# Performance work log

Hardware: AMD Instinct MI355X
Metric: run time of the kernel (lower is better)

Reference implementation:

```python
import jax, jax.numpy as jnp
import numpy as np

N_HEADS = 4
D_K = 64
SCALE = D_K ** (-0.5)


def setup_inputs() -> dict:
    key = jax.random.key(0)
    k1, k2, k3, k4, k5 = jax.random.split(key, 5)
    B, C, H, W = 16, 256, 32, 32
    x = jax.random.normal(k1, (B, C, H, W), dtype=jnp.float32)
    # Linear weights stored as (in, out) for x @ W convention
    w_qkv = jax.random.normal(k2, (C, N_HEADS * D_K * 3), dtype=jnp.float32) * (C ** -0.5)
    b_qkv = jax.random.normal(k3, (N_HEADS * D_K * 3,), dtype=jnp.float32) * 0.02
    w_out = jax.random.normal(k4, (N_HEADS * D_K, C), dtype=jnp.float32) * ((N_HEADS * D_K) ** -0.5)
    b_out = jax.random.normal(k5, (C,), dtype=jnp.float32) * 0.02
    return {"x": x, "w_qkv": w_qkv, "b_qkv": b_qkv, "w_out": w_out, "b_out": b_out}


def reference(x, w_qkv, b_qkv, w_out, b_out):
    # NOTE: the original torch module defines GroupNorm but never applies it
    # in forward; we faithfully reproduce the forward as written.
    B, C, H, W = x.shape
    S = H * W
    xs = x.reshape(B, C, S).transpose(0, 2, 1)            # [B, S, C]
    qkv = (xs @ w_qkv + b_qkv).reshape(B, S, N_HEADS, 3 * D_K)
    q, k, v = jnp.split(qkv, 3, axis=-1)                   # each [B, S, H, d_k]
    attn = jnp.einsum('bihd,bjhd->bijh', q, k) * SCALE     # [B, S, S, H]
    attn = jax.nn.softmax(attn, axis=2)                    # softmax over j (keys)
    res = jnp.einsum('bijh,bjhd->bihd', attn, v)           # [B, S, H, d_k]
    res = res.reshape(B, S, N_HEADS * D_K)
    res = res @ w_out + b_out + xs                         # residual add
    return res.transpose(0, 2, 1).reshape(B, C, H, W)
```

## Files before the change

### kernel.cpp

```cpp
#include <hip/hip_runtime.h>
#include <hip/hip_bf16.h>

typedef __attribute__((ext_vector_type(8))) short short8;
typedef __attribute__((ext_vector_type(4))) short short4v;
typedef __attribute__((ext_vector_type(4))) float floatx4;
typedef unsigned short u16;

#define SCL_LOG2E 0.1803368801111204f

__device__ inline u16 f2b(float f) {
  __hip_bfloat16 h = __float2bfloat16(f);
  union { __hip_bfloat16 h; u16 u; } cv; cv.h = h; return cv.u;
}
__device__ inline float b2f(u16 u) {
  union { u16 u; __hip_bfloat16 h; } cv; cv.u = u; return __bfloat162float(cv.h);
}

__global__ __launch_bounds__(256) void tr_f32_bf16(const float* __restrict__ in,
                                                   u16* __restrict__ out, int R, int Cc) {
  __shared__ u16 tile[32][33];
  int bz = blockIdx.z;
  const float* inb = in + (size_t)bz * R * Cc;
  u16* outb = out + (size_t)bz * R * Cc;
  int c0 = blockIdx.x * 32, r0 = blockIdx.y * 32;
  int tx = threadIdx.x, ty = threadIdx.y;
#pragma unroll
  for (int i = 0; i < 32; i += 8)
    tile[ty + i][tx] = f2b(inb[(size_t)(r0 + ty + i) * Cc + c0 + tx]);
  __syncthreads();
#pragma unroll
  for (int i = 0; i < 32; i += 8)
    outb[(size_t)(c0 + ty + i) * R + r0 + tx] = tile[tx][ty + i];
}

__global__ __launch_bounds__(256) void tr64_f32_bf16(const float* __restrict__ in,
                                                     u16* __restrict__ out,
                                                     int R, int Cc) {
  __shared__ u16 tile[64][72];
  int bz = blockIdx.z;
  const float* inb = in + (size_t)bz * R * Cc;
  u16* outb = out + (size_t)bz * R * Cc;
  int c0 = blockIdx.x * 64, r0 = blockIdx.y * 64;
  int tx = threadIdx.x, ty = threadIdx.y;
#pragma unroll
  for (int i = 0; i < 4; i++) {
    int r = ty + 16 * i;
    float4 v = *(const float4*)&inb[(size_t)(r0 + r) * Cc + c0 + tx * 4];
    tile[tx * 4 + 0][r] = f2b(v.x);
    tile[tx * 4 + 1][r] = f2b(v.y);
    tile[tx * 4 + 2][r] = f2b(v.z);
    tile[tx * 4 + 3][r] = f2b(v.w);
  }
  __syncthreads();
#pragma unroll
  for (int i = 0; i < 4; i++) {
    int cc = ty + 16 * i;
    ushort4 o = *(ushort4*)&tile[cc][tx * 4];
    *(ushort4*)&outb[(size_t)(c0 + cc) * R + r0 + tx * 4] = o;
  }
}

__global__ __launch_bounds__(256) void qkv_gemm(const u16* __restrict__ xs,
                                                const u16* __restrict__ wT,
                                                const float* __restrict__ bias,
                                                u16* __restrict__ Qo,
                                                u16* __restrict__ Ko,
                                                u16* __restrict__ Vto) {
  __shared__ u16 As[128 * 32];
  __shared__ u16 Bs[128 * 32];
  const int tid = threadIdx.x, wave = tid >> 6, lane = tid & 63;
  const int l15 = lane & 15, quad = lane >> 4;
  const int wm = (wave >> 1) * 64, wn = (wave & 1) * 64;
  const int m0 = blockIdx.x * 128, n0 = blockIdx.y * 128;

  floatx4 acc[4][4] = {};
  const int srow = wave * 32 + (lane >> 2);
  const int scol = (lane & 3) * 8;

  for (int kt = 0; kt < 256; kt += 32) {
#pragma unroll
    for (int i = 0; i < 2; i++) {
      int r = srow + i * 16;
      *(short8*)&As[r * 32 + scol] =
          *(const short8*)&xs[(size_t)(m0 + r) * 256 + kt + scol];
      *(short8*)&Bs[r * 32 + scol] =
          *(const short8*)&wT[(size_t)(n0 + r) * 256 + kt + scol];
    }
    __syncthreads();
    short8 af[4], bfr[4];
#pragma unroll
    for (int mi = 0; mi < 4; mi++)
      af[mi] = *(short8*)&As[(wm + mi * 16 + l15) * 32 + quad * 8];
#pragma unroll
    for (int ni = 0; ni < 4; ni++)
      bfr[ni] = *(short8*)&Bs[(wn + ni * 16 + l15) * 32 + quad * 8];
#pragma unroll
    for (int mi = 0; mi < 4; mi++)
#pragma unroll
      for (int ni = 0; ni < 4; ni++)
        acc[mi][ni] = __builtin_amdgcn_mfma_f32_16x16x32_bf16(af[mi], bfr[ni],
                                                              acc[mi][ni], 0, 0, 0);
    __syncthreads();
  }

#pragma unroll
  for (int ni = 0; ni < 4; ni++) {
    int n = n0 + wn + ni * 16 + l15;
    float bv = bias[n];
    int h = n / 192;
    int rem = n - h * 192;
#pragma unroll
    for (int mi = 0; mi < 4; mi++) {
      int gm = m0 + wm + mi * 16 + quad * 4;
      int bb = gm >> 10, s = gm & 1023;
      if (rem < 128) {
        u16* dst;
        float scl;
        if (rem < 64) { dst = Qo; scl = SCL_LOG2E; } else { dst = Ko; scl = 1.0f; }
        int d = rem & 63;
#pragma unroll
        for (int r = 0; r < 4; r++)
          dst[((size_t)(bb * 4 + h) * 1024 + s + r) * 64 + d] =
              f2b((acc[mi][ni][r] + bv) * scl);
      } else {
        int d = rem - 128;
        ushort4 pk;
        pk.x = f2b(acc[mi][ni][0] + bv);
        pk.y = f2b(acc[mi][ni][1] + bv);
        pk.z = f2b(acc[mi][ni][2] + bv);
        pk.w = f2b(acc[mi][ni][3] + bv);
        *(ushort4*)&Vto[((size_t)(bb * 4 + h) * 64 + d) * 1024 + s] = pk;
      }
    }
  }
}

__global__ __launch_bounds__(256, 4) void attn_kern(const u16* __restrict__ Q,
                                                    const u16* __restrict__ K,
                                                    const u16* __restrict__ Vt,
                                                    u16* __restrict__ O) {
  __shared__ u16 kv[2 * 2 * 64 * 72];
  const int bh = blockIdx.y;
  const u16* Qp = Q + (size_t)bh * 64 * 1024;
  const u16* Kp = K + (size_t)bh * 64 * 1024;
  const u16* Vp = Vt + (size_t)bh * 64 * 1024;
  u16* Op = O + (size_t)bh * 64 * 1024;
  const int q0 = blockIdx.x * 64;
  const int tid = threadIdx.x, wave = tid >> 6, lane = tid & 63;
  const int l15 = lane & 15, quad = lane >> 4;

  short8 qa[2];
#pragma unroll
  for (int ks = 0; ks < 2; ks++)
    qa[ks] = *(const short8*)&Qp[(size_t)(q0 + wave * 16 + l15) * 64 + ks * 32 + quad * 8];

  const int srow = tid >> 2;
  const int sc = (tid & 3) * 16;

  {
    short8 k0 = *(const short8*)&Kp[(size_t)srow * 64 + sc];
    short8 k1 = *(const short8*)&Kp[(size_t)srow * 64 + sc + 8];
    short8 v0 = *(const short8*)&Vp[(size_t)srow * 1024 + sc];
    short8 v1 = *(const short8*)&Vp[(size_t)srow * 1024 + sc + 8];
    *(short8*)&kv[srow * 72 + sc] = k0;
    *(short8*)&kv[srow * 72 + sc + 8] = k1;
    *(short8*)&kv[4608 + srow * 72 + sc] = v0;
    *(short8*)&kv[4608 + srow * 72 + sc + 8] = v1;
  }
  __syncthreads();

  float lsum = 0.f;
  floatx4 acc[4] = {};

  for (int t = 0; t < 16; t++) {
    const u16* Ksb = kv + (t & 1) * 9216;
    const u16* Vsb = Ksb + 4608;

    short8 nk0, nk1, nv0, nv1;
    if (t < 15) {
      nk0 = *(const short8*)&Kp[(size_t)((t + 1) * 64 + srow) * 64 + sc];
      nk1 = *(const short8*)&Kp[(size_t)((t + 1) * 64 + srow) * 64 + sc + 8];
      nv0 = *(const short8*)&Vp[(size_t)srow * 1024 + (t + 1) * 64 + sc];
      nv1 = *(const short8*)&Vp[(size_t)srow * 1024 + (t + 1) * 64 + sc + 8];
    }

    floatx4 sf[4];
#pragma unroll
    for (int mj = 0; mj < 4; mj++) {
      short8 kb0 = *(const short8*)&Ksb[(mj * 16 + l15) * 72 + quad * 8];
      short8 kb1 = *(const short8*)&Ksb[(mj * 16 + l15) * 72 + 32 + quad * 8];
      floatx4 z = {};
      z = __builtin_amdgcn_mfma_f32_16x16x32_bf16(kb0, qa[0], z, 0, 0, 0);
      sf[mj] = __builtin_amdgcn_mfma_f32_16x16x32_bf16(kb1, qa[1], z, 0, 0, 0);
    }

    short4v pb[4];
#pragma unroll
    for (int mj = 0; mj < 4; mj++) {
      float p0 = exp2f(sf[mj][0]), p1 = exp2f(sf[mj][1]);
      float p2 = exp2f(sf[mj][2]), p3 = exp2f(sf[mj][3]);
      lsum += (p0 + p1) + (p2 + p3);
      short4v pk;
      pk[0] = (short)f2b(p0); pk[1] = (short)f2b(p1);
      pk[2] = (short)f2b(p2); pk[3] = (short)f2b(p3);
      pb[mj] = pk;
    }

#pragma unroll
    for (int c = 0; c < 4; c++)
#pragma unroll
      for (int md = 0; md < 4; md++) {
        short4v va = *(const short4v*)&Vsb[(md * 16 + l15) * 72 + c * 16 + quad * 4];
        acc[md] = __builtin_amdgcn_mfma_f32_16x16x16bf16_1k(va, pb[c], acc[md], 0, 0, 0);
      }

    if (t < 15) {
      u16* dst = kv + ((t + 1) & 1) * 9216;
      *(short8*)&dst[srow * 72 + sc] = nk0;
      *(short8*)&dst[srow * 72 + sc + 8] = nk1;
      *(short8*)&dst[4608 + srow * 72 + sc] = nv0;
      *(short8*)&dst[4608 + srow * 72 + sc + 8] = nv1;
    }
    __syncthreads();
  }

  lsum += __shfl_xor(lsum, 16, 64);
  lsum += __shfl_xor(lsum, 32, 64);
  float inv = 1.f / lsum;

  __syncthreads();
  u16* Ot = kv;
#pragma unroll
  for (int md = 0; md < 4; md++) {
    uint2 pk;
    u16 a0 = f2b(acc[md][0] * inv), a1 = f2b(acc[md][1] * inv);
    u16 a2 = f2b(acc[md][2] * inv), a3 = f2b(acc[md][3] * inv);
    pk.x = (unsigned)a0 | ((unsigned)a1 << 16);
    pk.y = (unsigned)a2 | ((unsigned)a3 << 16);
    *(uint2*)&Ot[(wave * 16 + l15) * 72 + md * 16 + quad * 4] = pk;
  }
#pragma unroll
  for (int h = 0; h < 2; h++) {
    int row = h * 8 + (lane >> 3);
    int col = (lane & 7) * 8;
    short8 v = *(const short8*)&Ot[(wave * 16 + row) * 72 + col];
    *(short8*)&Op[(size_t)(q0 + wave * 16 + row) * 64 + col] = v;
  }
}

__global__ __launch_bounds__(256) void out_gemm(const u16* __restrict__ Oin,
                                                const u16* __restrict__ wT,
                                                const float* __restrict__ bias,
                                                const float* __restrict__ x,
                                                float* __restrict__ out) {
  __shared__ u16 As[128 * 32];
  __shared__ u16 Bs[128 * 32];
  const int tid = threadIdx.x, wave = tid >> 6, lane = tid & 63;
  const int l15 = lane & 15, quad = lane >> 4;
  const int wm = (wave >> 1) * 64, wn = (wave & 1) * 64;
  const int m0 = blockIdx.x * 128, n0 = blockIdx.y * 128;
  const int bb = m0 >> 10;

  floatx4 acc[4][4] = {};
  const int srow = wave * 32 + (lane >> 2);
  const int scol = (lane & 3) * 8;

  for (int kt = 0; kt < 256; kt += 32) {
    int h = kt >> 6, d0 = kt & 63;
#pragma unroll
    for (int i = 0; i < 2; i++) {
      int r = srow + i * 16;
      int s = (m0 + r) & 1023;
      *(short8*)&As[r * 32 + scol] =
          *(const short8*)&Oin[((size_t)(bb * 4 + h) * 1024 + s) * 64 + d0 + scol];
      *(short8*)&Bs[r * 32 + scol] =
          *(const short8*)&wT[(size_t)(n0 + r) * 256 + kt + scol];
    }
    __syncthreads();
    short8 af[4], bfr[4];
#pragma unroll
    for (int mi = 0; mi < 4; mi++)
      af[mi] = *(short8*)&As[(wm + mi * 16 + l15) * 32 + quad * 8];
#pragma unroll
    for (int ni = 0; ni < 4; ni++)
      bfr[ni] = *(short8*)&Bs[(wn + ni * 16 + l15) * 32 + quad * 8];
#pragma unroll
    for (int mi = 0; mi < 4; mi++)
#pragma unroll
      for (int ni = 0; ni < 4; ni++)
        acc[mi][ni] = __builtin_amdgcn_mfma_f32_16x16x32_bf16(af[mi], bfr[ni],
                                                              acc[mi][ni], 0, 0, 0);
    __syncthreads();
  }

#pragma unroll
  for (int ni = 0; ni < 4; ni++) {
    int c = n0 + wn + ni * 16 + l15;
    float bv = bias[c];
#pragma unroll
    for (int mi = 0; mi < 4; mi++) {
      int gm = m0 + wm + mi * 16 + quad * 4;
      int s = gm & 1023;
      size_t idx = ((size_t)bb * 256 + c) * 1024 + s;
      float4 xr = *(const float4*)&x[idx];
      float4 o;
      o.x = acc[mi][ni][0] + bv + xr.x;
      o.y = acc[mi][ni][1] + bv + xr.y;
      o.z = acc[mi][ni][2] + bv + xr.z;
      o.w = acc[mi][ni][3] + bv + xr.w;
      *(float4*)&out[idx] = o;
    }
  }
}

extern "C" void kernel_launch(void* const* d_in, const int* in_sizes, int n_in,
                              void* d_out, int out_size, void* d_ws, size_t ws_size,
                              hipStream_t stream) {
  const float* x     = (const float*)d_in[0];
  const float* w_qkv = (const float*)d_in[1];
  const float* b_qkv = (const float*)d_in[2];
  const float* w_out = (const float*)d_in[3];
  const float* b_out = (const float*)d_in[4];
  float* out = (float*)d_out;
  char* ws = (char*)d_ws;

  u16* xs    = (u16*)(ws);
  u16* wqkvT = (u16*)(ws + 8388608);
  u16* woutT = (u16*)(ws + 8388608 + 393216);
  u16* Qb    = (u16*)(ws + 8912896);
  u16* Kb    = (u16*)(ws + 8912896 + 8388608);
  u16* Vtb   = (u16*)(ws + 8912896 + 16777216);
  u16* Ob    = xs;

  tr64_f32_bf16<<<dim3(16, 4, 16), dim3(16, 16), 0, stream>>>(x, xs, 256, 1024);
  tr_f32_bf16<<<dim3(24, 8, 1), dim3(32, 8), 0, stream>>>(w_qkv, wqkvT, 256, 768);
  tr_f32_bf16<<<dim3(8, 8, 1), dim3(32, 8), 0, stream>>>(w_out, woutT, 256, 256);
  qkv_gemm<<<dim3(128, 6), 256, 0, stream>>>(xs, wqkvT, b_qkv, Qb, Kb, Vtb);
  attn_kern<<<dim3(16, 64), 256, 0, stream>>>(Qb, Kb, Vtb, Ob);
  out_gemm<<<dim3(128, 2), 256, 0, stream>>>(Ob, woutT, b_out, x, out);
}
```

Before: 145.0 us.

## Fuse fp32-to-bf16 transposes into GEMMs and double per-wave query rows in attention

Removes the three standalone transpose/convert kernels. The QKV and output GEMMs now read fp32 x and the weights directly, converting to bf16 and transposing into padded shared memory inside the load loop. The attention kernel now processes 32 query rows per wave (128 per block), so each K/V tile loaded into LDS is reused for twice as many queries; launch bounds drop to 2 blocks per SM. The output GEMM uses 64-row tiles to launch more blocks. In exchange, more registers are used in attention, and GEMM loads become scalar LDS scatter stores that may hit bank conflicts.

```diff
diff --git a/kernel.cpp b/kernel.cpp
--- a/kernel.cpp
+++ b/kernel.cpp
@@ -12,88 +12,49 @@
   __hip_bfloat16 h = __float2bfloat16(f);
   union { __hip_bfloat16 h; u16 u; } cv; cv.h = h; return cv.u;
 }
-__device__ inline float b2f(u16 u) {
-  union { u16 u; __hip_bfloat16 h; } cv; cv.u = u; return __bfloat162float(cv.h);
-}
-
-__global__ __launch_bounds__(256) void tr_f32_bf16(const float* __restrict__ in,
-                                                   u16* __restrict__ out, int R, int Cc) {
-  __shared__ u16 tile[32][33];
-  int bz = blockIdx.z;
-  const float* inb = in + (size_t)bz * R * Cc;
-  u16* outb = out + (size_t)bz * R * Cc;
-  int c0 = blockIdx.x * 32, r0 = blockIdx.y * 32;
-  int tx = threadIdx.x, ty = threadIdx.y;
-#pragma unroll
-  for (int i = 0; i < 32; i += 8)
-    tile[ty + i][tx] = f2b(inb[(size_t)(r0 + ty + i) * Cc + c0 + tx]);
-  __syncthreads();
-#pragma unroll
-  for (int i = 0; i < 32; i += 8)
-    outb[(size_t)(c0 + ty + i) * R + r0 + tx] = tile[tx][ty + i];
-}
-
-__global__ __launch_bounds__(256) void tr64_f32_bf16(const float* __restrict__ in,
-                                                     u16* __restrict__ out,
-                                                     int R, int Cc) {
-  __shared__ u16 tile[64][72];
-  int bz = blockIdx.z;
-  const float* inb = in + (size_t)bz * R * Cc;
-  u16* outb = out + (size_t)bz * R * Cc;
-  int c0 = blockIdx.x * 64, r0 = blockIdx.y * 64;
-  int tx = threadIdx.x, ty = threadIdx.y;
-#pragma unroll
-  for (int i = 0; i < 4; i++) {
-    int r = ty + 16 * i;
-    float4 v = *(const float4*)&inb[(size_t)(r0 + r) * Cc + c0 + tx * 4];
-    tile[tx * 4 + 0][r] = f2b(v.x);
-    tile[tx * 4 + 1][r] = f2b(v.y);
-    tile[tx * 4 + 2][r] = f2b(v.z);
-    tile[tx * 4 + 3][r] = f2b(v.w);
-  }
-  __syncthreads();
-#pragma unroll
-  for (int i = 0; i < 4; i++) {
-    int cc = ty + 16 * i;
-    ushort4 o = *(ushort4*)&tile[cc][tx * 4];
-    *(ushort4*)&outb[(size_t)(c0 + cc) * R + r0 + tx * 4] = o;
-  }
-}
-
-__global__ __launch_bounds__(256) void qkv_gemm(const u16* __restrict__ xs,
-                                                const u16* __restrict__ wT,
+
+__global__ __launch_bounds__(256) void qkv_gemm(const float* __restrict__ x,
+                                                const float* __restrict__ wq,
                                                 const float* __restrict__ bias,
                                                 u16* __restrict__ Qo,
                                                 u16* __restrict__ Ko,
                                                 u16* __restrict__ Vto) {
-  __shared__ u16 As[128 * 32];
-  __shared__ u16 Bs[128 * 32];
+  __shared__ u16 As[128 * 40];
+  __shared__ u16 Bs[128 * 40];
   const int tid = threadIdx.x, wave = tid >> 6, lane = tid & 63;
   const int l15 = lane & 15, quad = lane >> 4;
   const int wm = (wave >> 1) * 64, wn = (wave & 1) * 64;
   const int m0 = blockIdx.x * 128, n0 = blockIdx.y * 128;
+  const int bb = m0 >> 10, s0 = m0 & 1023;
+  const int cl = tid >> 3, u = tid & 7;
 
   floatx4 acc[4][4] = {};
-  const int srow = wave * 32 + (lane >> 2);
-  const int scol = (lane & 3) * 8;
 
   for (int kt = 0; kt < 256; kt += 32) {
-#pragma unroll
-    for (int i = 0; i < 2; i++) {
-      int r = srow + i * 16;
-      *(short8*)&As[r * 32 + scol] =
-          *(const short8*)&xs[(size_t)(m0 + r) * 256 + kt + scol];
-      *(short8*)&Bs[r * 32 + scol] =
-          *(const short8*)&wT[(size_t)(n0 + r) * 256 + kt + scol];
+    const float* xr = x + ((size_t)(bb * 256 + kt + cl)) * 1024 + s0;
+    const float* wr = wq + (size_t)(kt + cl) * 768 + n0;
+#pragma unroll
+    for (int j = 0; j < 4; j++) {
+      int e = u * 4 + 32 * j;
+      float4 va = *(const float4*)&xr[e];
+      float4 vb = *(const float4*)&wr[e];
+      As[(e + 0) * 40 + cl] = f2b(va.x);
+      As[(e + 1) * 40 + cl] = f2b(va.y);
+      As[(e + 2) * 40 + cl] = f2b(va.z);
+      As[(e + 3) * 40 + cl] = f2b(va.w);
+      Bs[(e + 0) * 40 + cl] = f2b(vb.x);
+      Bs[(e + 1) * 40 + cl] = f2b(vb.y);
+      Bs[(e + 2) * 40 + cl] = f2b(vb.z);
+      Bs[(e + 3) * 40 + cl] = f2b(vb.w);
     }
     __syncthreads();
     short8 af[4], bfr[4];
 #pragma unroll
     for (int mi = 0; mi < 4; mi++)
-      af[mi] = *(short8*)&As[(wm + mi * 16 + l15) * 32 + quad * 8];
+      af[mi] = *(short8*)&As[(wm + mi * 16 + l15) * 40 + quad * 8];
 #pragma unroll
     for (int ni = 0; ni < 4; ni++)
-      bfr[ni] = *(short8*)&Bs[(wn + ni * 16 + l15) * 32 + quad * 8];
+      bfr[ni] = *(short8*)&Bs[(wn + ni * 16 + l15) * 40 + quad * 8];
 #pragma unroll
     for (int mi = 0; mi < 4; mi++)
 #pragma unroll
@@ -112,7 +73,7 @@
 #pragma unroll
     for (int mi = 0; mi < 4; mi++) {
       int gm = m0 + wm + mi * 16 + quad * 4;
-      int bb = gm >> 10, s = gm & 1023;
+      int s = gm & 1023;
       if (rem < 128) {
         u16* dst;
         float scl;
@@ -135,7 +96,7 @@
   }
 }
 
-__global__ __launch_bounds__(256, 4) void attn_kern(const u16* __restrict__ Q,
+__global__ __launch_bounds__(256, 2) void attn_kern(const u16* __restrict__ Q,
                                                     const u16* __restrict__ K,
                                                     const u16* __restrict__ Vt,
                                                     u16* __restrict__ O) {
@@ -145,14 +106,17 @@
   const u16* Kp = K + (size_t)bh * 64 * 1024;
   const u16* Vp = Vt + (size_t)bh * 64 * 1024;
   u16* Op = O + (size_t)bh * 64 * 1024;
-  const int q0 = blockIdx.x * 64;
+  const int q0 = blockIdx.x * 128;
   const int tid = threadIdx.x, wave = tid >> 6, lane = tid & 63;
   const int l15 = lane & 15, quad = lane >> 4;
 
-  short8 qa[2];
-#pragma unroll
-  for (int ks = 0; ks < 2; ks++)
-    qa[ks] = *(const short8*)&Qp[(size_t)(q0 + wave * 16 + l15) * 64 + ks * 32 + quad * 8];
+  short8 qa[2][2];
+#pragma unroll
+  for (int qi = 0; qi < 2; qi++)
+#pragma unroll
+    for (int kh = 0; kh < 2; kh++)
+      qa[qi][kh] = *(const short8*)&Qp[(size_t)(q0 + wave * 32 + qi * 16 + l15) * 64 +
+                                       kh * 32 + quad * 8];
 
   const int srow = tid >> 2;
   const int sc = (tid & 3) * 16;
@@ -169,8 +133,8 @@
   }
   __syncthreads();
 
-  float lsum = 0.f;
-  floatx4 acc[4] = {};
+  float lsum[2] = {0.f, 0.f};
+  floatx4 acc[2][4] = {};
 
   for (int t = 0; t < 16; t++) {
     const u16* Ksb = kv + (t & 1) * 9216;
@@ -184,34 +148,48 @@
       nv1 = *(const short8*)&Vp[(size_t)srow * 1024 + (t + 1) * 64 + sc + 8];
     }
 
-    floatx4 sf[4];
-#pragma unroll
-    for (int mj = 0; mj < 4; mj++) {
-      short8 kb0 = *(const short8*)&Ksb[(mj * 16 + l15) * 72 + quad * 8];
-      short8 kb1 = *(const short8*)&Ksb[(mj * 16 + l15) * 72 + 32 + quad * 8];
-      floatx4 z = {};
-      z = __builtin_amdgcn_mfma_f32_16x16x32_bf16(kb0, qa[0], z, 0, 0, 0);
-      sf[mj] = __builtin_amdgcn_mfma_f32_16x16x32_bf16(kb1, qa[1], z, 0, 0, 0);
-    }
-
-    short4v pb[4];
-#pragma unroll
-    for (int mj = 0; mj < 4; mj++) {
-      float p0 = exp2f(sf[mj][0]), p1 = exp2f(sf[mj][1]);
-      float p2 = exp2f(sf[mj][2]), p3 = exp2f(sf[mj][3]);
-      lsum += (p0 + p1) + (p2 + p3);
-      short4v pk;
-      pk[0] = (short)f2b(p0); pk[1] = (short)f2b(p1);
-      pk[2] = (short)f2b(p2); pk[3] = (short)f2b(p3);
-      pb[mj] = pk;
-    }
+    short8 kb[4][2];
+#pragma unroll
+    for (int mj = 0; mj < 4; mj++)
+#pragma unroll
+      for (int kh = 0; kh < 2; kh++)
+        kb[mj][kh] = *(const short8*)&Ksb[(mj * 16 + l15) * 72 + kh * 32 + quad * 8];
+
+    floatx4 sf[2][4];
+#pragma unroll
+    for (int qi = 0; qi < 2; qi++)
+#pragma unroll
+      for (int mj = 0; mj < 4; mj++) {
+        floatx4 z = {};
+        z = __builtin_amdgcn_mfma_f32_16x16x32_bf16(kb[mj][0], qa[qi][0], z, 0, 0, 0);
+        sf[qi][mj] =
+            __builtin_amdgcn_mfma_f32_16x16x32_bf16(kb[mj][1], qa[qi][1], z, 0, 0, 0);
+      }
+
+    short4v pb[2][4];
+#pragma unroll
+    for (int qi = 0; qi < 2; qi++)
+#pragma unroll
+      for (int mj = 0; mj < 4; mj++) {
+        float p0 = exp2f(sf[qi][mj][0]), p1 = exp2f(sf[qi][mj][1]);
+        float p2 = exp2f(sf[qi][mj][2]), p3 = exp2f(sf[qi][mj][3]);
+        lsum[qi] += (p0 + p1) + (p2 + p3);
+        short4v pk;
+        pk[0] = (short)f2b(p0); pk[1] = (short)f2b(p1);
+        pk[2] = (short)f2b(p2); pk[3] = (short)f2b(p3);
+        pb[qi][mj] = pk;
+      }
 
 #pragma unroll
     for (int c = 0; c < 4; c++)
 #pragma unroll
       for (int md = 0; md < 4; md++) {
         short4v va = *(const short4v*)&Vsb[(md * 16 + l15) * 72 + c * 16 + quad * 4];
-        acc[md] = __builtin_amdgcn_mfma_f32_16x16x16bf16_1k(va, pb[c], acc[md], 0, 0, 0);
+#pragma unroll
+        for (int qi = 0; qi < 2; qi++)
+          acc[qi][md] =
+              __builtin_amdgcn_mfma_f32_16x16x16bf16_1k(va, pb[qi][c], acc[qi][md],
+                                                        0, 0, 0);
       }
 
     if (t < 15) {
@@ -224,68 +202,78 @@
     __syncthreads();
   }
 
-  lsum += __shfl_xor(lsum, 16, 64);
-  lsum += __shfl_xor(lsum, 32, 64);
-  float inv = 1.f / lsum;
+  float inv[2];
+#pragma unroll
+  for (int qi = 0; qi < 2; qi++) {
+    lsum[qi] += __shfl_xor(lsum[qi], 16, 64);
+    lsum[qi] += __shfl_xor(lsum[qi], 32, 64);
+    inv[qi] = 1.f / lsum[qi];
+  }
 
   __syncthreads();
   u16* Ot = kv;
 #pragma unroll
-  for (int md = 0; md < 4; md++) {
-    uint2 pk;
-    u16 a0 = f2b(acc[md][0] * inv), a1 = f2b(acc[md][1] * inv);
-    u16 a2 = f2b(acc[md][2] * inv), a3 = f2b(acc[md][3] * inv);
-    pk.x = (unsigned)a0 | ((unsigned)a1 << 16);
-    pk.y = (unsigned)a2 | ((unsigned)a3 << 16);
-    *(uint2*)&Ot[(wave * 16 + l15) * 72 + md * 16 + quad * 4] = pk;
-  }
-#pragma unroll
-  for (int h = 0; h < 2; h++) {
-    int row = h * 8 + (lane >> 3);
+  for (int qi = 0; qi < 2; qi++)
+#pragma unroll
+    for (int md = 0; md < 4; md++) {
+      uint2 pk;
+      u16 a0 = f2b(acc[qi][md][0] * inv[qi]), a1 = f2b(acc[qi][md][1] * inv[qi]);
+      u16 a2 = f2b(acc[qi][md][2] * inv[qi]), a3 = f2b(acc[qi][md][3] * inv[qi]);
+      pk.x = (unsigned)a0 | ((unsigned)a1 << 16);
+      pk.y = (unsigned)a2 | ((unsigned)a3 << 16);
+      *(uint2*)&Ot[(wave * 32 + qi * 16 + l15) * 72 + md * 16 + quad * 4] = pk;
+    }
+  __syncthreads();
+#pragma unroll
+  for (int rr = 0; rr < 4; rr++) {
+    int row = wave * 32 + (lane >> 3) + 8 * rr;
     int col = (lane & 7) * 8;
-    short8 v = *(const short8*)&Ot[(wave * 16 + row) * 72 + col];
-    *(short8*)&Op[(size_t)(q0 + wave * 16 + row) * 64 + col] = v;
+    short8 v = *(const short8*)&Ot[row * 72 + col];
+    *(short8*)&Op[(size_t)(q0 + row) * 64 + col] = v;
   }
 }
 
 __global__ __launch_bounds__(256) void out_gemm(const u16* __restrict__ Oin,
-                                                const u16* __restrict__ wT,
+                                                const float* __restrict__ wo,
                                                 const float* __restrict__ bias,
                                                 const float* __restrict__ x,
                                                 float* __restrict__ out) {
-  __shared__ u16 As[128 * 32];
-  __shared__ u16 Bs[128 * 32];
+  __shared__ u16 As[64 * 32];
+  __shared__ u16 Bs[128 * 40];
   const int tid = threadIdx.x, wave = tid >> 6, lane = tid & 63;
   const int l15 = lane & 15, quad = lane >> 4;
-  const int wm = (wave >> 1) * 64, wn = (wave & 1) * 64;
-  const int m0 = blockIdx.x * 128, n0 = blockIdx.y * 128;
-  const int bb = m0 >> 10;
-
-  floatx4 acc[4][4] = {};
-  const int srow = wave * 32 + (lane >> 2);
-  const int scol = (lane & 3) * 8;
+  const int wm = (wave >> 1) * 32, wn = (wave & 1) * 64;
+  const int m0 = blockIdx.x * 64, n0 = blockIdx.y * 128;
+  const int bb = m0 >> 10, s0 = m0 & 1023;
+  const int ar = tid >> 2, ach = (tid & 3) * 8;
+  const int cl = tid >> 3, u = tid & 7;
+
+  floatx4 acc[2][4] = {};
 
   for (int kt = 0; kt < 256; kt += 32) {
     int h = kt >> 6, d0 = kt & 63;
-#pragma unroll
-    for (int i = 0; i < 2; i++) {
-      int r = srow + i * 16;
-      int s = (m0 + r) & 1023;
-      *(short8*)&As[r * 32 + scol] =
-          *(const short8*)&Oin[((size_t)(bb * 4 + h) * 1024 + s) * 64 + d0 + scol];
-      *(short8*)&Bs[r * 32 + scol] =
-          *(const short8*)&wT[(size_t)(n0 + r) * 256 + kt + scol];
-    }
-    __syncthreads();
-    short8 af[4], bfr[4];
-#pragma unroll
-    for (int mi = 0; mi < 4; mi++)
+    *(short8*)&As[ar * 32 + ach] =
+        *(const short8*)&Oin[((size_t)(bb * 4 + h) * 1024 + s0 + ar) * 64 + d0 + ach];
+    const float* wr = wo + (size_t)(kt + cl) * 256 + n0;
+#pragma unroll
+    for (int j = 0; j < 4; j++) {
+      int e = u * 4 + 32 * j;
+      float4 vb = *(const float4*)&wr[e];
+      Bs[(e + 0) * 40 + cl] = f2b(vb.x);
+      Bs[(e + 1) * 40 + cl] = f2b(vb.y);
+      Bs[(e + 2) * 40 + cl] = f2b(vb.z);
+      Bs[(e + 3) * 40 + cl] = f2b(vb.w);
+    }
+    __syncthreads();
+    short8 af[2], bfr[4];
+#pragma unroll
+    for (int mi = 0; mi < 2; mi++)
       af[mi] = *(short8*)&As[(wm + mi * 16 + l15) * 32 + quad * 8];
 #pragma unroll
     for (int ni = 0; ni < 4; ni++)
-      bfr[ni] = *(short8*)&Bs[(wn + ni * 16 + l15) * 32 + quad * 8];
-#pragma unroll
-    for (int mi = 0; mi < 4; mi++)
+      bfr[ni] = *(short8*)&Bs[(wn + ni * 16 + l15) * 40 + quad * 8];
+#pragma unroll
+    for (int mi = 0; mi < 2; mi++)
 #pragma unroll
       for (int ni = 0; ni < 4; ni++)
         acc[mi][ni] = __builtin_amdgcn_mfma_f32_16x16x32_bf16(af[mi], bfr[ni],
@@ -298,7 +286,7 @@
     int c = n0 + wn + ni * 16 + l15;
     float bv = bias[c];
 #pragma unroll
-    for (int mi = 0; mi < 4; mi++) {
+    for (int mi = 0; mi < 2; mi++) {
       int gm = m0 + wm + mi * 16 + quad * 4;
       int s = gm & 1023;
       size_t idx = ((size_t)bb * 256 + c) * 1024 + s;
@@ -324,18 +312,12 @@
   float* out = (float*)d_out;
   char* ws = (char*)d_ws;
 
-  u16* xs    = (u16*)(ws);
-  u16* wqkvT = (u16*)(ws + 8388608);
-  u16* woutT = (u16*)(ws + 8388608 + 393216);
-  u16* Qb    = (u16*)(ws + 8912896);
-  u16* Kb    = (u16*)(ws + 8912896 + 8388608);
-  u16* Vtb   = (u16*)(ws + 8912896 + 16777216);
-  u16* Ob    = xs;
-
-  tr64_f32_bf16<<<dim3(16, 4, 16), dim3(16, 16), 0, stream>>>(x, xs, 256, 1024);
-  tr_f32_bf16<<<dim3(24, 8, 1), dim3(32, 8), 0, stream>>>(w_qkv, wqkvT, 256, 768);
-  tr_f32_bf16<<<dim3(8, 8, 1), dim3(32, 8), 0, stream>>>(w_out, woutT, 256, 256);
-  qkv_gemm<<<dim3(128, 6), 256, 0, stream>>>(xs, wqkvT, b_qkv, Qb, Kb, Vtb);
-  attn_kern<<<dim3(16, 64), 256, 0, stream>>>(Qb, Kb, Vtb, Ob);
-  out_gemm<<<dim3(128, 2), 256, 0, stream>>>(Ob, woutT, b_out, x, out);
-}
+  u16* Qb  = (u16*)(ws);
+  u16* Kb  = (u16*)(ws + 8388608);
+  u16* Vtb = (u16*)(ws + 16777216);
+  u16* Ob  = (u16*)(ws + 25165824);
+
+  qkv_gemm<<<dim3(128, 6), 256, 0, stream>>>(x, w_qkv, b_qkv, Qb, Kb, Vtb);
+  attn_kern<<<dim3(8, 64), 256, 0, stream>>>(Qb, Kb, Vtb, Ob);
+  out_gemm<<<dim3(256, 2), 256, 0, stream>>>(Ob, w_out, b_out, x, out);
+}
```

Measured after the change: 143.7 us. No clear change (-0.9%).
